# Kernel tuning notes

Measured on AMD Instinct MI355X. Metric: run time of the kernel, lower is better.

The kernel has to match this reference:

```python
import jax, jax.numpy as jnp
import numpy as np

TEMP = 0.07
POS_WINDOW = 2
EPS = 1e-8
NEG = -1e9  # finite large-negative for masking (safe under vjp)


def _l2norm(x):
    # matches F.normalize(dim=-1) with eps=1e-12
    n = jnp.sqrt(jnp.sum(x * x, axis=-1, keepdims=True))
    return x / jnp.maximum(n, 1e-12)


def setup_inputs() -> dict:
    key = jax.random.key(0)
    k1, k2, k3, k4, k5 = jax.random.split(key, 5)
    B, T, D = 32, 1024, 256
    eeg_enc = jax.random.normal(k1, (B, T, D), dtype=jnp.float32)
    eye_enc = jax.random.normal(k2, (B, T, D), dtype=jnp.float32)
    mask = jax.random.randint(k3, (B, T), 0, 2, dtype=jnp.int32)
    W_eeg = jax.random.normal(k4, (D, D), dtype=jnp.float32) / np.sqrt(D)
    W_eye = jax.random.normal(k5, (D, D), dtype=jnp.float32) / np.sqrt(D)
    return {"eeg_enc": eeg_enc, "eye_enc": eye_enc, "mask": mask,
            "W_eeg": W_eeg, "W_eye": W_eye}


def reference(eeg_enc, eye_enc, mask, W_eeg, W_eye):
    B, T, D = eeg_enc.shape
    valid = mask > 0  # (B,T)
    # nn.Linear(bias=False): x @ W.T, then L2-normalize
    e = _l2norm(jnp.einsum('btd,ed->bte', eeg_enc, W_eeg))
    v = _l2norm(jnp.einsum('btd,ed->bte', eye_enc, W_eye))
    sims = jnp.einsum('bid,bjd->bij', e, v) / TEMP  # (B,T,T)
    # rank of each valid step within the compressed (gathered) ordering
    rank = jnp.cumsum(valid.astype(jnp.int32), axis=-1) - 1  # (B,T)
    band = jnp.abs(rank[:, :, None] - rank[:, None, :]) <= POS_WINDOW
    pair = valid[:, :, None] & valid[:, None, :]  # both steps valid
    pos = pair & band
    # per-row max over positive (banded) entries
    pos_scores = jnp.max(jnp.where(pos, sims, NEG), axis=-1)  # (B,T)
    # logsumexp over valid columns (the gathered sims row)
    lse = jax.nn.logsumexp(jnp.where(valid[:, None, :], sims, NEG), axis=-1)
    row_loss = -(pos_scores - lse)  # (B,T)
    Tv = jnp.sum(valid, axis=-1)  # (B,)
    per_b = jnp.sum(jnp.where(valid, row_loss, 0.0), axis=-1) / jnp.maximum(Tv, 1)
    per_b = jnp.where(Tv >= 2, per_b, 0.0)  # skip samples with <2 valid steps
    return jnp.sum(per_b) / (B + EPS)
```

## Files before the change

### kernel.cpp

```cpp
#include <hip/hip_runtime.h>
#include <hip/hip_bf16.h>

typedef __attribute__((ext_vector_type(8))) short bf16x8;
typedef __attribute__((ext_vector_type(4))) float f32x4;

#define INVT (1.0f/0.07f)

static __device__ __forceinline__ short f2bf(float f){
    unsigned int u = __float_as_uint(f);
    unsigned int r = (u + 0x7fffu + ((u >> 16) & 1u)) >> 16;
    return (short)r;
}
static __device__ __forceinline__ float bf2f(short s){
    return __uint_as_float(((unsigned int)(unsigned short)s) << 16);
}

static __device__ __forceinline__ void gld16(const void* g, void* l){
    __builtin_amdgcn_global_load_lds(
        (const __attribute__((address_space(1))) unsigned int*)g,
        (__attribute__((address_space(3))) unsigned int*)l, 16, 0, 0);
}

__global__ __launch_bounds__(256) void prep_kernel(const float* __restrict__ Weeg,
                                                   const float* __restrict__ Weye,
                                                   const int* __restrict__ mask,
                                                   short* __restrict__ Wout,
                                                   int* __restrict__ rank,
                                                   int* __restrict__ idx,
                                                   int* __restrict__ Tv,
                                                   float* __restrict__ cb){
    __shared__ int ssum[256];
    int tid = threadIdx.x;
    if (blockIdx.x < 512){
        int i = blockIdx.x * 256 + tid;
        float v = (i < 65536) ? Weeg[i] : Weye[i - 65536];
        Wout[i] = f2bf(v);
        return;
    }
    int b = blockIdx.x - 512;
    int local[4]; int s = 0;
    #pragma unroll
    for (int q = 0; q < 4; ++q){
        int t = tid*4 + q;
        local[q] = (mask[b*1024 + t] > 0) ? 1 : 0;
        s += local[q];
    }
    ssum[tid] = s;
    __syncthreads();
    for (int off = 1; off < 256; off <<= 1){
        int add = (tid >= off) ? ssum[tid - off] : 0;
        __syncthreads();
        ssum[tid] += add;
        __syncthreads();
    }
    int run = ssum[tid] - s;
    #pragma unroll
    for (int q = 0; q < 4; ++q){
        int t = tid*4 + q;
        int g = b*1024 + t;
        run += local[q];
        rank[g] = run - 1;
        cb[g]   = local[q] ? 0.0f : -1e9f;
        if (local[q]) idx[b*1024 + run - 1] = t;
    }
    if (tid == 255) Tv[b] = ssum[255];
}

__global__ __launch_bounds__(256, 3) void proj_kernel(const float* __restrict__ Aeeg,
                                                      const float* __restrict__ Aeye,
                                                      const short* __restrict__ Wbf,
                                                      short* __restrict__ Eout,
                                                      short* __restrict__ Vout){
    __shared__ short sW[64 * 256];
    int sel = blockIdx.y;
    const float* A   = sel ? Aeye : Aeeg;
    const short* W   = Wbf + sel * 65536;
    short*       Out = sel ? Vout : Eout;

    int tid = threadIdx.x;
    int w = tid >> 6, lane = tid & 63;
    int l15 = lane & 15, lq = lane >> 4;
    int kb  = lq * 8;
    int row0 = blockIdx.x * 64;

    bf16x8 xf[8];
    {
        const float* ap = A + (size_t)(row0 + w*16 + l15) * 256 + kb;
        #pragma unroll
        for (int g = 0; g < 8; ++g){
            float4 x0 = *(const float4*)(ap + g*32);
            float4 x1 = *(const float4*)(ap + g*32 + 4);
            bf16x8 t;
            t[0]=f2bf(x0.x); t[1]=f2bf(x0.y); t[2]=f2bf(x0.z); t[3]=f2bf(x0.w);
            t[4]=f2bf(x1.x); t[5]=f2bf(x1.y); t[6]=f2bf(x1.z); t[7]=f2bf(x1.w);
            xf[g] = t;
        }
    }

    f32x4 acc[16];
    #pragma unroll
    for (int q = 0; q < 16; ++q) acc[q] = (f32x4){0.f,0.f,0.f,0.f};

    int ro   = lane >> 5;
    int cb_s = lane & 31;
    int s7   = l15 & 7;

    #pragma unroll
    for (int pass = 0; pass < 4; ++pass){
        if (pass) __syncthreads();
        #pragma unroll
        for (int p = 0; p < 8; ++p){
            int rl  = w*16 + p*2 + ro;
            int cbg = cb_s ^ ((p*2 + ro) & 7);
            gld16(W + (size_t)(pass*64 + rl)*256 + cbg*8,
                  &sW[(w*16 + p*2) * 256]);
        }
        __syncthreads();
        #pragma unroll
        for (int nt = 0; nt < 4; ++nt){
            f32x4 c = acc[pass*4 + nt];
            int rbase = (nt*16 + l15) * 256;
            #pragma unroll
            for (int g = 0; g < 8; ++g){
                bf16x8 wf = *(const bf16x8*)&sW[rbase + (((g*4 + lq) ^ s7) << 3)];
                c = __builtin_amdgcn_mfma_f32_16x16x32_bf16(wf, xf[g], c, 0, 0, 0);
            }
            acc[pass*4 + nt] = c;
        }
    }

    float ss = 0.f;
    #pragma unroll
    for (int q = 0; q < 16; ++q){
        #pragma unroll
        for (int r = 0; r < 4; ++r){ float x = acc[q][r]; ss += x*x; }
    }
    ss += __shfl_xor(ss, 16);
    ss += __shfl_xor(ss, 32);
    float scale = 1.0f / fmaxf(sqrtf(ss), 1e-12f);

    short* op = Out + (size_t)(row0 + w*16 + l15) * 256 + lq*4;
    #pragma unroll
    for (int q = 0; q < 16; ++q){
        short4 pk;
        pk.x = f2bf(acc[q][0] * scale);
        pk.y = f2bf(acc[q][1] * scale);
        pk.z = f2bf(acc[q][2] * scale);
        pk.w = f2bf(acc[q][3] * scale);
        *(short4*)(op + ((q >> 2) * 64 + (q & 3) * 16)) = pk;
    }
}

__global__ __launch_bounds__(256, 4) void loss_kernel(const short* __restrict__ E,
                                                      const short* __restrict__ V,
                                                      const float* __restrict__ cb,
                                                      float* __restrict__ psum){
    __shared__ short sE[128 * 64];
    __shared__ short sV[128 * 64];

    int i0 = blockIdx.x * 128;
    int j0 = blockIdx.y * 128;
    int b  = blockIdx.z;

    int tid = threadIdx.x;
    int w = tid >> 6, lane = tid & 63;
    int wi = w >> 1, wj = w & 1;
    int l15 = lane & 15, lq = lane >> 4;
    int s7 = l15 & 7;

    int swz = ((lane & 7) ^ (lane >> 3)) * 8;
    const short* Eg = E + ((size_t)b*1024 + i0 + w*32 + (lane>>3))*256 + swz;
    const short* Vg = V + ((size_t)b*1024 + j0 + w*32 + (lane>>3))*256 + swz;
    short* sEw = &sE[(w*32)*64];
    short* sVw = &sV[(w*32)*64];

    float cbv[4];
    #pragma unroll
    for (int jj = 0; jj < 4; ++jj)
        cbv[jj] = cb[b*1024 + j0 + wj*64 + jj*16 + l15];

    f32x4 acc[4][4];
    #pragma unroll
    for (int ii = 0; ii < 4; ++ii)
        #pragma unroll
        for (int jj = 0; jj < 4; ++jj) acc[ii][jj] = (f32x4){0.f,0.f,0.f,0.f};

    #pragma unroll
    for (int kc = 0; kc < 4; ++kc){
        __syncthreads();
        #pragma unroll
        for (int p = 0; p < 4; ++p){
            gld16(Eg + kc*64 + p*2048, sEw + p*512);
            gld16(Vg + kc*64 + p*2048, sVw + p*512);
        }
        __syncthreads();

        #pragma unroll
        for (int ks = 0; ks < 2; ++ks){
            bf16x8 af[4], bf[4];
            #pragma unroll
            for (int t = 0; t < 4; ++t){
                int co = (((ks*4 + lq) ^ s7)) << 3;
                af[t] = *(const bf16x8*)&sE[(wi*64 + t*16 + l15)*64 + co];
                bf[t] = *(const bf16x8*)&sV[(wj*64 + t*16 + l15)*64 + co];
            }
            #pragma unroll
            for (int ii = 0; ii < 4; ++ii)
                #pragma unroll
                for (int jj = 0; jj < 4; ++jj)
                    acc[ii][jj] = __builtin_amdgcn_mfma_f32_16x16x32_bf16(af[ii], bf[jj], acc[ii][jj], 0, 0, 0);
        }
    }

    float ls[4][4];
    #pragma unroll
    for (int ii = 0; ii < 4; ++ii){
        #pragma unroll
        for (int r = 0; r < 4; ++r){
            float s = 0.f;
            #pragma unroll
            for (int jj = 0; jj < 4; ++jj)
                s += __expf(fmaf(acc[ii][jj][r], INVT, cbv[jj]));
            ls[ii][r] = s;
        }
    }
    #pragma unroll
    for (int ii = 0; ii < 4; ++ii){
        #pragma unroll
        for (int r = 0; r < 4; ++r){
            float v = ls[ii][r];
            v += __shfl_xor(v, 1);
            v += __shfl_xor(v, 2);
            v += __shfl_xor(v, 4);
            v += __shfl_xor(v, 8);
            ls[ii][r] = v;
        }
    }
    if (l15 == 0){
        float* pp = psum + (((size_t)(b*16 + blockIdx.y*2 + wj)) << 10);
        int ibase = i0 + wi*64 + lq*4;
        #pragma unroll
        for (int ii = 0; ii < 4; ++ii){
            #pragma unroll
            for (int r = 0; r < 4; ++r)
                pp[ibase + ii*16 + r] = ls[ii][r];
        }
    }
}

__global__ __launch_bounds__(256) void pos_kernel(const short* __restrict__ E,
                                                  const short* __restrict__ V,
                                                  const int* __restrict__ mask,
                                                  const int* __restrict__ rank,
                                                  const int* __restrict__ idx,
                                                  const int* __restrict__ Tv,
                                                  float* __restrict__ pmax){
    int tid = threadIdx.x;
    int gl  = tid & 15;
    int rf  = (blockIdx.x * 256 + tid) >> 4;
    int b   = rf >> 10;
    if (mask[rf] <= 0) return;

    int ri = rank[rf];
    int tv = Tv[b];
    int lo = ri - 2; if (lo < 0) lo = 0;
    int hi = ri + 2; if (hi > tv - 1) hi = tv - 1;

    const short* epp = E + (size_t)rf * 256 + gl * 16;
    float ev[16];
    {
        bf16x8 e0 = *(const bf16x8*)epp;
        bf16x8 e1 = *(const bf16x8*)(epp + 8);
        #pragma unroll
        for (int k = 0; k < 8; ++k){ ev[k] = bf2f(e0[k]); ev[8+k] = bf2f(e1[k]); }
    }
    float pm = -1e30f;
    for (int r = lo; r <= hi; ++r){
        int j = idx[b*1024 + r];
        const short* vpp = V + ((size_t)(b*1024) + j) * 256 + gl * 16;
        bf16x8 v0 = *(const bf16x8*)vpp;
        bf16x8 v1 = *(const bf16x8*)(vpp + 8);
        float s = 0.f;
        #pragma unroll
        for (int k = 0; k < 8; ++k){
            s = fmaf(ev[k],   bf2f(v0[k]), s);
            s = fmaf(ev[8+k], bf2f(v1[k]), s);
        }
        s += __shfl_xor(s, 1);
        s += __shfl_xor(s, 2);
        s += __shfl_xor(s, 4);
        s += __shfl_xor(s, 8);
        pm = fmaxf(pm, s);
    }
    if (gl == 0) pmax[rf] = pm * INVT;
}

__global__ __launch_bounds__(256) void reduce_kernel(const float* __restrict__ psum,
                                                     const float* __restrict__ pmax,
                                                     const int* __restrict__ mask,
                                                     const int* __restrict__ Tv,
                                                     float* __restrict__ per_b){
    __shared__ float sred[4];
    int b = blockIdx.x, tid = threadIdx.x;
    float a = 0.f;
    const float* pp = psum + ((size_t)b << 14);
    #pragma unroll
    for (int q = 0; q < 4; ++q){
        int i = q*256 + tid;
        int g = b*1024 + i;
        if (mask[g] > 0){
            float ps = 0.f;
            #pragma unroll
            for (int s = 0; s < 16; ++s) ps += pp[i + (s << 10)];
            a += logf(ps) - pmax[g];
        }
    }
    #pragma unroll
    for (int m = 1; m < 64; m <<= 1) a += __shfl_xor(a, m);
    if ((tid & 63) == 0) sred[tid >> 6] = a;
    __syncthreads();
    if (tid == 0){
        float t = sred[0] + sred[1] + sred[2] + sred[3];
        int tv = Tv[b];
        per_b[b] = (tv >= 2) ? t / (float)tv : 0.f;
    }
}

__global__ void final_kernel(const float* __restrict__ per_b,
                             float* __restrict__ out){
    int tid = threadIdx.x;
    float v = (tid < 32) ? per_b[tid] : 0.f;
    #pragma unroll
    for (int m = 1; m < 64; m <<= 1) v += __shfl_xor(v, m);
    if (tid == 0) out[0] = v / 32.0f;
}

extern "C" void kernel_launch(void* const* d_in, const int* in_sizes, int n_in,
                              void* d_out, int out_size, void* d_ws, size_t ws_size,
                              hipStream_t stream) {
    const float* eeg  = (const float*)d_in[0];
    const float* eye  = (const float*)d_in[1];
    const int*   mask = (const int*)d_in[2];
    const float* Weeg = (const float*)d_in[3];
    const float* Weye = (const float*)d_in[4];
    float* out = (float*)d_out;

    char* ws = (char*)d_ws;
    short* e_bf  = (short*)(ws);
    short* v_bf  = (short*)(ws + 16777216);
    short* wbf   = (short*)(ws + 33554432);
    int*   rank  = (int*)  (ws + 33816576);
    int*   idx   = (int*)  (ws + 33947648);
    float* cb    = (float*)(ws + 34078720);
    float* psum  = (float*)(ws + 34209792);
    float* pmax  = (float*)(ws + 36306944);
    int*   Tv    = (int*)  (ws + 36438016);
    float* per_b = (float*)(ws + 36438144);

    prep_kernel<<<544, 256, 0, stream>>>(Weeg, Weye, mask, wbf, rank, idx, Tv, cb);
    proj_kernel<<<dim3(512, 2), 256, 0, stream>>>(eeg, eye, wbf, e_bf, v_bf);
    loss_kernel<<<dim3(8, 8, 32), 256, 0, stream>>>(e_bf, v_bf, cb, psum);
    pos_kernel<<<2048, 256, 0, stream>>>(e_bf, v_bf, mask, rank, idx, Tv, pmax);
    reduce_kernel<<<32, 256, 0, stream>>>(psum, pmax, mask, Tv, per_b);
    final_kernel<<<1, 64, 0, stream>>>(per_b, out);
}
```

Before: 170.5 us.

## Transpose partial-sum layout, widen reduce grid with atomics, raise occupancy bounds

```diff
diff --git a/kernel.cpp b/kernel.cpp
--- a/kernel.cpp
+++ b/kernel.cpp
@@ -28,7 +28,8 @@
                                                    int* __restrict__ rank,
                                                    int* __restrict__ idx,
                                                    int* __restrict__ Tv,
-                                                   float* __restrict__ cb){
+                                                   float* __restrict__ cb,
+                                                   float* __restrict__ bsum){
     __shared__ int ssum[256];
     int tid = threadIdx.x;
     if (blockIdx.x < 512){
@@ -38,6 +39,7 @@
         return;
     }
     int b = blockIdx.x - 512;
+    if (tid == 0) bsum[b] = 0.f;
     int local[4]; int s = 0;
     #pragma unroll
     for (int q = 0; q < 4; ++q){
@@ -66,7 +68,7 @@
     if (tid == 255) Tv[b] = ssum[255];
 }
 
-__global__ __launch_bounds__(256, 3) void proj_kernel(const float* __restrict__ Aeeg,
+__global__ __launch_bounds__(256, 5) void proj_kernel(const float* __restrict__ Aeeg,
                                                       const float* __restrict__ Aeye,
                                                       const short* __restrict__ Wbf,
                                                       short* __restrict__ Eout,
@@ -151,7 +153,7 @@
     }
 }
 
-__global__ __launch_bounds__(256, 4) void loss_kernel(const short* __restrict__ E,
+__global__ __launch_bounds__(256, 5) void loss_kernel(const short* __restrict__ E,
                                                       const short* __restrict__ V,
                                                       const float* __restrict__ cb,
                                                       float* __restrict__ psum){
@@ -237,13 +239,14 @@
         }
     }
     if (l15 == 0){
-        float* pp = psum + (((size_t)(b*16 + blockIdx.y*2 + wj)) << 10);
+        int slice = blockIdx.y*2 + wj;
         int ibase = i0 + wi*64 + lq*4;
+        float* pp = psum + (((size_t)b << 10) << 4);
         #pragma unroll
         for (int ii = 0; ii < 4; ++ii){
             #pragma unroll
             for (int r = 0; r < 4; ++r)
-                pp[ibase + ii*16 + r] = ls[ii][r];
+                pp[(size_t)(ibase + ii*16 + r)*16 + slice] = ls[ii][r];
         }
     }
 }
@@ -298,38 +301,32 @@
 __global__ __launch_bounds__(256) void reduce_kernel(const float* __restrict__ psum,
                                                      const float* __restrict__ pmax,
                                                      const int* __restrict__ mask,
-                                                     const int* __restrict__ Tv,
-                                                     float* __restrict__ per_b){
-    __shared__ float sred[4];
-    int b = blockIdx.x, tid = threadIdx.x;
+                                                     float* __restrict__ bsum){
+    int b  = blockIdx.x >> 2;
+    int i  = (blockIdx.x & 3) * 256 + threadIdx.x;
+    int g  = b*1024 + i;
     float a = 0.f;
-    const float* pp = psum + ((size_t)b << 14);
-    #pragma unroll
-    for (int q = 0; q < 4; ++q){
-        int i = q*256 + tid;
-        int g = b*1024 + i;
-        if (mask[g] > 0){
-            float ps = 0.f;
-            #pragma unroll
-            for (int s = 0; s < 16; ++s) ps += pp[i + (s << 10)];
-            a += logf(ps) - pmax[g];
-        }
+    if (mask[g] > 0){
+        const float* pp = psum + ((size_t)g << 4);
+        float ps = 0.f;
+        #pragma unroll
+        for (int s = 0; s < 16; ++s) ps += pp[s];
+        a = logf(ps) - pmax[g];
     }
     #pragma unroll
     for (int m = 1; m < 64; m <<= 1) a += __shfl_xor(a, m);
-    if ((tid & 63) == 0) sred[tid >> 6] = a;
-    __syncthreads();
-    if (tid == 0){
-        float t = sred[0] + sred[1] + sred[2] + sred[3];
-        int tv = Tv[b];
-        per_b[b] = (tv >= 2) ? t / (float)tv : 0.f;
-    }
-}
-
-__global__ void final_kernel(const float* __restrict__ per_b,
+    if ((threadIdx.x & 63) == 0 && a != 0.f) atomicAdd(&bsum[b], a);
+}
+
+__global__ void final_kernel(const float* __restrict__ bsum,
+                             const int* __restrict__ Tv,
                              float* __restrict__ out){
     int tid = threadIdx.x;
-    float v = (tid < 32) ? per_b[tid] : 0.f;
+    float v = 0.f;
+    if (tid < 32){
+        int tv = Tv[tid];
+        if (tv >= 2) v = bsum[tid] / (float)tv;
+    }
     #pragma unroll
     for (int m = 1; m < 64; m <<= 1) v += __shfl_xor(v, m);
     if (tid == 0) out[0] = v / 32.0f;
@@ -355,12 +352,12 @@
     float* psum  = (float*)(ws + 34209792);
     float* pmax  = (float*)(ws + 36306944);
     int*   Tv    = (int*)  (ws + 36438016);
-    float* per_b = (float*)(ws + 36438144);
-
-    prep_kernel<<<544, 256, 0, stream>>>(Weeg, Weye, mask, wbf, rank, idx, Tv, cb);
+    float* bsum  = (float*)(ws + 36438144);
+
+    prep_kernel<<<544, 256, 0, stream>>>(Weeg, Weye, mask, wbf, rank, idx, Tv, cb, bsum);
     proj_kernel<<<dim3(512, 2), 256, 0, stream>>>(eeg, eye, wbf, e_bf, v_bf);
     loss_kernel<<<dim3(8, 8, 32), 256, 0, stream>>>(e_bf, v_bf, cb, psum);
     pos_kernel<<<2048, 256, 0, stream>>>(e_bf, v_bf, mask, rank, idx, Tv, pmax);
-    reduce_kernel<<<32, 256, 0, stream>>>(psum, pmax, mask, Tv, per_b);
-    final_kernel<<<1, 64, 0, stream>>>(per_b, out);
-}
+    reduce_kernel<<<128, 256, 0, stream>>>(psum, pmax, mask, bsum);
+    final_kernel<<<1, 64, 0, stream>>>(bsum, Tv, out);
+}
```

After: 209.2 us. 22.7% more time.
